# Kernel tuning notes

Measured on AMD Instinct MI355X. Metric: run time of the kernel, lower is better.

Reference implementation:

```python
import jax, jax.numpy as jnp
import numpy as np

T_FRAMES = 8
BN_EPS = 1e-3


def _depthwise_conv1d(x, w, b):
    # x: (M, C, T), w: (C, 1, 3) depthwise kernel, b: (C,)
    C = x.shape[1]
    y = jax.lax.conv_general_dilated(
        x, w, window_strides=(1,), padding=[(1, 1)],
        feature_group_count=C,
        dimension_numbers=("NCH", "OIH", "NCH"))
    return y + b[None, :, None]


def setup_inputs() -> dict:
    key = jax.random.key(0)
    ks = jax.random.split(key, 12)
    C, Cr = 64, 16  # dim, dim // TEA_ratio
    NT, H, W = 128, 56, 56
    inp = {
        "x": jax.random.normal(ks[0], (NT, C, H, W), dtype=jnp.float32),
        # depthwise temporal convs (Conv1d, groups=C, k=3)
        "shift_w": jax.random.normal(ks[1], (C, 1, 3), dtype=jnp.float32) * 0.3,
        "shift_b": jax.random.normal(ks[2], (C,), dtype=jnp.float32) * 0.1,
        "gate_w": jax.random.normal(ks[3], (C, 1, 3), dtype=jnp.float32) * 0.3,
        "gate_b": jax.random.normal(ks[4], (C,), dtype=jnp.float32) * 0.1,
        # BatchNorm1d (eval-mode running stats)
        "bn_gamma": jnp.ones((C,), dtype=jnp.float32),
        "bn_beta": jnp.zeros((C,), dtype=jnp.float32),
        "bn_mean": jax.random.normal(ks[5], (C,), dtype=jnp.float32) * 0.1,
        "bn_var": jax.random.uniform(ks[6], (C,), dtype=jnp.float32, minval=0.5, maxval=1.5),
        # TEA 1x1 convs stored as dense matrices
        "sq_w": jax.random.normal(ks[7], (Cr, C), dtype=jnp.float32) * 0.1,
        "sq_b": jax.random.normal(ks[8], (Cr,), dtype=jnp.float32) * 0.1,
        "ex_w": jax.random.normal(ks[9], (C, Cr), dtype=jnp.float32) * 0.1,
        "ex_b": jax.random.normal(ks[10], (C,), dtype=jnp.float32) * 0.1,
    }
    return inp


def reference(x, shift_w, shift_b, gate_w, gate_b,
              bn_gamma, bn_beta, bn_mean, bn_var,
              sq_w, sq_b, ex_w, ex_b):
    NT, C, H, W = x.shape
    T = T_FRAMES
    N = NT // T
    Cr = sq_w.shape[0]

    # ---- MotionExcitation ----
    # 1x1 squeeze conv: (NT, C, H, W) -> (NT, Cr, H, W)
    xs = jnp.einsum("nchw,kc->nkhw", x, sq_w) + sq_b[None, :, None, None]
    xr = xs.reshape(N, T, Cr, H, W)
    # diff = first frame - frames[:-1], zero-padded at the end (as in source)
    diff = xr[:, :1] - xr[:, :-1]                      # (N, T-1, Cr, H, W)
    diff = jnp.concatenate(
        [diff, jnp.zeros((N, 1, Cr, H, W), dtype=x.dtype)], axis=1)
    diff = diff.reshape(NT, Cr, H, W)
    gap = diff.mean(axis=(2, 3))                       # (NT, Cr)  global avg pool
    att = jax.nn.sigmoid(gap @ ex_w.T + ex_b)          # (NT, C)   expand + sigmoid
    S = x * att[:, :, None, None] + x                  # residual * att + residual

    # ---- Learnable temporal shift ----
    def to_ct(z):
        # (NT, C, H, W) -> (N, T, C, H, W) -> (N, H, W, C, T) -> (N*H*W, C, T)
        return z.reshape(N, T, C, H, W).transpose(0, 3, 4, 2, 1).reshape(-1, C, T)

    Sc = _depthwise_conv1d(to_ct(S), shift_w, shift_b)
    Gc = _depthwise_conv1d(to_ct(x), gate_w, gate_b)
    inv = bn_gamma * jax.lax.rsqrt(bn_var + BN_EPS)
    Gc = (Gc - bn_mean[None, :, None]) * inv[None, :, None] + bn_beta[None, :, None]
    out = Sc * jax.nn.sigmoid(Gc)                      # (N*H*W, C, T)

    out = out.reshape(N, H, W, C, T).transpose(0, 4, 3, 1, 2).reshape(NT, C, H, W)
    return out
```

## Files before the change

### kernel.cpp

```cpp
#include <hip/hip_runtime.h>
#include <math.h>

#define CDIM 64
#define CR 16
#define TFR 8
#define NBATCH 16
#define NTOT 128
#define HWPIX 3136
#define HW4 784

__global__ __launch_bounds__(256) void spatial_mean_kernel(
    const float* __restrict__ x, float* __restrict__ xbar) {
  const int b = blockIdx.x;
  const float4* xp = reinterpret_cast<const float4*>(x + (size_t)b * HWPIX);
  float s = 0.f;
  for (int i = threadIdx.x; i < HW4; i += 256) {
    float4 v = xp[i];
    s += (v.x + v.y) + (v.z + v.w);
  }
  #pragma unroll
  for (int off = 32; off > 0; off >>= 1) s += __shfl_down(s, off, 64);
  __shared__ float wsum[4];
  const int lane = threadIdx.x & 63, wid = threadIdx.x >> 6;
  if (lane == 0) wsum[wid] = s;
  __syncthreads();
  if (threadIdx.x == 0) {
    float tot = (wsum[0] + wsum[1]) + (wsum[2] + wsum[3]);
    xbar[b] = tot * (1.0f / (float)HWPIX);
  }
}

__global__ __launch_bounds__(64) void att_kernel(
    const float* __restrict__ xbar,
    const float* __restrict__ sq_w,
    const float* __restrict__ ex_w,
    const float* __restrict__ ex_b,
    float* __restrict__ attp1) {
  const int nt = blockIdx.x;
  const int n = nt >> 3;
  const int t = nt & 7;
  const int c = threadIdx.x;
  __shared__ float d[CDIM];
  __shared__ float gap[CR];
  d[c] = (t == TFR - 1) ? 0.f
                        : (xbar[(n * TFR) * CDIM + c] - xbar[nt * CDIM + c]);
  __syncthreads();
  if (c < CR) {
    float g = 0.f;
    #pragma unroll
    for (int cc = 0; cc < CDIM; ++cc) g += sq_w[c * CDIM + cc] * d[cc];
    gap[c] = g;
  }
  __syncthreads();
  float a = ex_b[c];
  #pragma unroll
  for (int k = 0; k < CR; ++k) a += ex_w[c * CR + k] * gap[k];
  attp1[nt * CDIM + c] = 1.f + 1.f / (1.f + __expf(-a));
}

__global__ __launch_bounds__(256) void fused_shift_kernel(
    const float* __restrict__ x,
    const float* __restrict__ attp1,
    const float* __restrict__ shift_w, const float* __restrict__ shift_b,
    const float* __restrict__ gate_w,  const float* __restrict__ gate_b,
    const float* __restrict__ bn_gamma, const float* __restrict__ bn_beta,
    const float* __restrict__ bn_mean,  const float* __restrict__ bn_var,
    float* __restrict__ out) {
  const int tid = blockIdx.x * 256 + threadIdx.x;
  const int q = tid % HW4;
  const int c = (tid / HW4) & (CDIM - 1);
  const int n = tid / (HW4 * CDIM);

  const float sw0 = shift_w[c * 3 + 0], sw1 = shift_w[c * 3 + 1],
              sw2 = shift_w[c * 3 + 2], sb = shift_b[c];
  const float inv = bn_gamma[c] * rsqrtf(bn_var[c] + 1e-3f);
  const float g0 = gate_w[c * 3 + 0] * inv, g1 = gate_w[c * 3 + 1] * inv,
              g2 = gate_w[c * 3 + 2] * inv;
  const float gbias = (gate_b[c] - bn_mean[c]) * inv + bn_beta[c];

  const size_t base = ((size_t)(n * TFR) * CDIM + c) * HWPIX + (size_t)q * 4;
  const size_t tstride = (size_t)CDIM * HWPIX;

  float4 xv[TFR], Sv[TFR];
  #pragma unroll
  for (int t = 0; t < TFR; ++t) {
    xv[t] = *reinterpret_cast<const float4*>(x + base + (size_t)t * tstride);
    const float a = attp1[(n * TFR + t) * CDIM + c];
    Sv[t].x = xv[t].x * a;
    Sv[t].y = xv[t].y * a;
    Sv[t].z = xv[t].z * a;
    Sv[t].w = xv[t].w * a;
  }

  const float4 zero4 = make_float4(0.f, 0.f, 0.f, 0.f);
  #pragma unroll
  for (int t = 0; t < TFR; ++t) {
    const float4 Sm = (t > 0) ? Sv[t - 1] : zero4;
    const float4 Sp = (t < TFR - 1) ? Sv[t + 1] : zero4;
    const float4 xm = (t > 0) ? xv[t - 1] : zero4;
    const float4 xp = (t < TFR - 1) ? xv[t + 1] : zero4;

    float4 o;
    {
      const float sc = sb + sw0 * Sm.x + sw1 * Sv[t].x + sw2 * Sp.x;
      const float gc = gbias + g0 * xm.x + g1 * xv[t].x + g2 * xp.x;
      o.x = sc * (1.f / (1.f + __expf(-gc)));
    }
    {
      const float sc = sb + sw0 * Sm.y + sw1 * Sv[t].y + sw2 * Sp.y;
      const float gc = gbias + g0 * xm.y + g1 * xv[t].y + g2 * xp.y;
      o.y = sc * (1.f / (1.f + __expf(-gc)));
    }
    {
      const float sc = sb + sw0 * Sm.z + sw1 * Sv[t].z + sw2 * Sp.z;
      const float gc = gbias + g0 * xm.z + g1 * xv[t].z + g2 * xp.z;
      o.z = sc * (1.f / (1.f + __expf(-gc)));
    }
    {
      const float sc = sb + sw0 * Sm.w + sw1 * Sv[t].w + sw2 * Sp.w;
      const float gc = gbias + g0 * xm.w + g1 * xv[t].w + g2 * xp.w;
      o.w = sc * (1.f / (1.f + __expf(-gc)));
    }
    *reinterpret_cast<float4*>(out + base + (size_t)t * tstride) = o;
  }
}

extern "C" void kernel_launch(void* const* d_in, const int* in_sizes, int n_in,
                              void* d_out, int out_size, void* d_ws, size_t ws_size,
                              hipStream_t stream) {
  const float* x        = (const float*)d_in[0];
  const float* shift_w  = (const float*)d_in[1];
  const float* shift_b  = (const float*)d_in[2];
  const float* gate_w   = (const float*)d_in[3];
  const float* gate_b   = (const float*)d_in[4];
  const float* bn_gamma = (const float*)d_in[5];
  const float* bn_beta  = (const float*)d_in[6];
  const float* bn_mean  = (const float*)d_in[7];
  const float* bn_var   = (const float*)d_in[8];
  const float* sq_w     = (const float*)d_in[9];
  const float* ex_w     = (const float*)d_in[11];
  const float* ex_b     = (const float*)d_in[12];
  float* out = (float*)d_out;

  float* xbar  = (float*)d_ws;
  float* attp1 = (float*)d_ws + NTOT * CDIM;

  spatial_mean_kernel<<<NTOT * CDIM, 256, 0, stream>>>(x, xbar);
  att_kernel<<<NTOT, CDIM, 0, stream>>>(xbar, sq_w, ex_w, ex_b, attp1);
  fused_shift_kernel<<<(NBATCH * CDIM * HW4) / 256, 256, 0, stream>>>(
      x, attp1, shift_w, shift_b, gate_w, gate_b,
      bn_gamma, bn_beta, bn_mean, bn_var, out);
}
```

Baseline: 54.83 us.

## Fuse attention MLP into shift kernel, one block per (n,c), nontemporal stores

Removes the separate att_kernel launch: each block of the shift kernel is now assigned one (batch, channel) pair and recomputes that batch's squeeze/expand attention vector into shared memory. Each block then loops over the 784 pixel quads, and the outputs use nontemporal stores. This saves one kernel launch and the attp1 round-trip through memory. In exchange, the small MLP is computed redundantly in every block, each block waits on two syncthreads before streaming starts, and the grid shrinks to 1024 blocks that each loop over about 3 iterations with a tail.

```diff
diff --git a/kernel.cpp b/kernel.cpp
--- a/kernel.cpp
+++ b/kernel.cpp
@@ -8,6 +8,8 @@
 #define NTOT 128
 #define HWPIX 3136
 #define HW4 784
+
+typedef float floatx4 __attribute__((ext_vector_type(4)));
 
 __global__ __launch_bounds__(256) void spatial_mean_kernel(
     const float* __restrict__ x, float* __restrict__ xbar) {
@@ -30,46 +32,47 @@
   }
 }
 
-__global__ __launch_bounds__(64) void att_kernel(
+__global__ __launch_bounds__(256) void fused_shift_kernel(
+    const float* __restrict__ x,
     const float* __restrict__ xbar,
     const float* __restrict__ sq_w,
     const float* __restrict__ ex_w,
     const float* __restrict__ ex_b,
-    float* __restrict__ attp1) {
-  const int nt = blockIdx.x;
-  const int n = nt >> 3;
-  const int t = nt & 7;
-  const int c = threadIdx.x;
-  __shared__ float d[CDIM];
-  __shared__ float gap[CR];
-  d[c] = (t == TFR - 1) ? 0.f
-                        : (xbar[(n * TFR) * CDIM + c] - xbar[nt * CDIM + c]);
-  __syncthreads();
-  if (c < CR) {
-    float g = 0.f;
-    #pragma unroll
-    for (int cc = 0; cc < CDIM; ++cc) g += sq_w[c * CDIM + cc] * d[cc];
-    gap[c] = g;
-  }
-  __syncthreads();
-  float a = ex_b[c];
-  #pragma unroll
-  for (int k = 0; k < CR; ++k) a += ex_w[c * CR + k] * gap[k];
-  attp1[nt * CDIM + c] = 1.f + 1.f / (1.f + __expf(-a));
-}
-
-__global__ __launch_bounds__(256) void fused_shift_kernel(
-    const float* __restrict__ x,
-    const float* __restrict__ attp1,
     const float* __restrict__ shift_w, const float* __restrict__ shift_b,
     const float* __restrict__ gate_w,  const float* __restrict__ gate_b,
     const float* __restrict__ bn_gamma, const float* __restrict__ bn_beta,
     const float* __restrict__ bn_mean,  const float* __restrict__ bn_var,
     float* __restrict__ out) {
-  const int tid = blockIdx.x * 256 + threadIdx.x;
-  const int q = tid % HW4;
-  const int c = (tid / HW4) & (CDIM - 1);
-  const int n = tid / (HW4 * CDIM);
+  const int n = blockIdx.x >> 6;
+  const int c = blockIdx.x & (CDIM - 1);
+  const int tid = threadIdx.x;
+
+  __shared__ float dsh[TFR][CDIM];
+  __shared__ float gap[TFR][CR];
+  __shared__ float attp1_sh[TFR];
+  {
+    const int base0 = (n * TFR) * CDIM;
+    for (int i = tid; i < TFR * CDIM; i += 256) {
+      const int t = i >> 6, cc = i & (CDIM - 1);
+      dsh[t][cc] = (t == TFR - 1) ? 0.f : (xbar[base0 + cc] - xbar[base0 + t * CDIM + cc]);
+    }
+  }
+  __syncthreads();
+  if (tid < TFR * CR) {
+    const int t = tid >> 4, k = tid & (CR - 1);
+    float g = 0.f;
+    #pragma unroll
+    for (int cc = 0; cc < CDIM; ++cc) g += sq_w[k * CDIM + cc] * dsh[t][cc];
+    gap[t][k] = g;
+  }
+  __syncthreads();
+  if (tid < TFR) {
+    float a = ex_b[c];
+    #pragma unroll
+    for (int k = 0; k < CR; ++k) a += ex_w[c * CR + k] * gap[tid][k];
+    attp1_sh[tid] = 1.f + 1.f / (1.f + __expf(-a));
+  }
+  __syncthreads();
 
   const float sw0 = shift_w[c * 3 + 0], sw1 = shift_w[c * 3 + 1],
               sw2 = shift_w[c * 3 + 2], sb = shift_b[c];
@@ -78,50 +81,55 @@
               g2 = gate_w[c * 3 + 2] * inv;
   const float gbias = (gate_b[c] - bn_mean[c]) * inv + bn_beta[c];
 
-  const size_t base = ((size_t)(n * TFR) * CDIM + c) * HWPIX + (size_t)q * 4;
+  float ap1[TFR];
+  #pragma unroll
+  for (int t = 0; t < TFR; ++t) ap1[t] = attp1_sh[t];
+
+  const size_t base_nc = ((size_t)(n * TFR) * CDIM + c) * HWPIX;
   const size_t tstride = (size_t)CDIM * HWPIX;
+  const float4 zero4 = make_float4(0.f, 0.f, 0.f, 0.f);
 
-  float4 xv[TFR], Sv[TFR];
-  #pragma unroll
-  for (int t = 0; t < TFR; ++t) {
-    xv[t] = *reinterpret_cast<const float4*>(x + base + (size_t)t * tstride);
-    const float a = attp1[(n * TFR + t) * CDIM + c];
-    Sv[t].x = xv[t].x * a;
-    Sv[t].y = xv[t].y * a;
-    Sv[t].z = xv[t].z * a;
-    Sv[t].w = xv[t].w * a;
-  }
-
-  const float4 zero4 = make_float4(0.f, 0.f, 0.f, 0.f);
-  #pragma unroll
-  for (int t = 0; t < TFR; ++t) {
-    const float4 Sm = (t > 0) ? Sv[t - 1] : zero4;
-    const float4 Sp = (t < TFR - 1) ? Sv[t + 1] : zero4;
-    const float4 xm = (t > 0) ? xv[t - 1] : zero4;
-    const float4 xp = (t < TFR - 1) ? xv[t + 1] : zero4;
-
-    float4 o;
-    {
-      const float sc = sb + sw0 * Sm.x + sw1 * Sv[t].x + sw2 * Sp.x;
-      const float gc = gbias + g0 * xm.x + g1 * xv[t].x + g2 * xp.x;
-      o.x = sc * (1.f / (1.f + __expf(-gc)));
+  for (int i = tid; i < HW4; i += 256) {
+    const size_t off = base_nc + (size_t)i * 4;
+    float4 xv[TFR], Sv[TFR];
+    #pragma unroll
+    for (int t = 0; t < TFR; ++t) {
+      xv[t] = *reinterpret_cast<const float4*>(x + off + (size_t)t * tstride);
+      Sv[t].x = xv[t].x * ap1[t];
+      Sv[t].y = xv[t].y * ap1[t];
+      Sv[t].z = xv[t].z * ap1[t];
+      Sv[t].w = xv[t].w * ap1[t];
     }
-    {
-      const float sc = sb + sw0 * Sm.y + sw1 * Sv[t].y + sw2 * Sp.y;
-      const float gc = gbias + g0 * xm.y + g1 * xv[t].y + g2 * xp.y;
-      o.y = sc * (1.f / (1.f + __expf(-gc)));
+    #pragma unroll
+    for (int t = 0; t < TFR; ++t) {
+      const float4 Sm = (t > 0) ? Sv[t - 1] : zero4;
+      const float4 Sp = (t < TFR - 1) ? Sv[t + 1] : zero4;
+      const float4 xm = (t > 0) ? xv[t - 1] : zero4;
+      const float4 xp = (t < TFR - 1) ? xv[t + 1] : zero4;
+      floatx4 o;
+      {
+        const float sc = sb + sw0 * Sm.x + sw1 * Sv[t].x + sw2 * Sp.x;
+        const float gc = gbias + g0 * xm.x + g1 * xv[t].x + g2 * xp.x;
+        o.x = sc * (1.f / (1.f + __expf(-gc)));
+      }
+      {
+        const float sc = sb + sw0 * Sm.y + sw1 * Sv[t].y + sw2 * Sp.y;
+        const float gc = gbias + g0 * xm.y + g1 * xv[t].y + g2 * xp.y;
+        o.y = sc * (1.f / (1.f + __expf(-gc)));
+      }
+      {
+        const float sc = sb + sw0 * Sm.z + sw1 * Sv[t].z + sw2 * Sp.z;
+        const float gc = gbias + g0 * xm.z + g1 * xv[t].z + g2 * xp.z;
+        o.z = sc * (1.f / (1.f + __expf(-gc)));
+      }
+      {
+        const float sc = sb + sw0 * Sm.w + sw1 * Sv[t].w + sw2 * Sp.w;
+        const float gc = gbias + g0 * xm.w + g1 * xv[t].w + g2 * xp.w;
+        o.w = sc * (1.f / (1.f + __expf(-gc)));
+      }
+      __builtin_nontemporal_store(
+          o, reinterpret_cast<floatx4*>(out + off + (size_t)t * tstride));
     }
-    {
-      const float sc = sb + sw0 * Sm.z + sw1 * Sv[t].z + sw2 * Sp.z;
-      const float gc = gbias + g0 * xm.z + g1 * xv[t].z + g2 * xp.z;
-      o.z = sc * (1.f / (1.f + __expf(-gc)));
-    }
-    {
-      const float sc = sb + sw0 * Sm.w + sw1 * Sv[t].w + sw2 * Sp.w;
-      const float gc = gbias + g0 * xm.w + g1 * xv[t].w + g2 * xp.w;
-      o.w = sc * (1.f / (1.f + __expf(-gc)));
-    }
-    *reinterpret_cast<float4*>(out + base + (size_t)t * tstride) = o;
   }
 }
 
@@ -142,12 +150,10 @@
   const float* ex_b     = (const float*)d_in[12];
   float* out = (float*)d_out;
 
-  float* xbar  = (float*)d_ws;
-  float* attp1 = (float*)d_ws + NTOT * CDIM;
+  float* xbar = (float*)d_ws;
 
   spatial_mean_kernel<<<NTOT * CDIM, 256, 0, stream>>>(x, xbar);
-  att_kernel<<<NTOT, CDIM, 0, stream>>>(xbar, sq_w, ex_w, ex_b, attp1);
-  fused_shift_kernel<<<(NBATCH * CDIM * HW4) / 256, 256, 0, stream>>>(
-      x, attp1, shift_w, shift_b, gate_w, gate_b,
+  fused_shift_kernel<<<NBATCH * CDIM, 256, 0, stream>>>(
+      x, xbar, sq_w, ex_w, ex_b, shift_w, shift_b, gate_w, gate_b,
       bn_gamma, bn_beta, bn_mean, bn_var, out);
 }
```

Measured after the change: 58.25 us. 6.2% more time.
